# Performance work log

Measured on AMD Instinct MI355X. Metric: run time of the kernel, lower is better.

Reference implementation:

```python
import jax, jax.numpy as jnp
import numpy as np

N = 100000   # nodes
E = 300000   # directed edges
D = 256      # emb_dim
G = 4000     # graphs
L = 5        # num_layer
F_IN = 40    # num_atom_features
NUM_BOND_TYPE = 6       # pretrain-gnns convention; self-loop bond type = 4
NUM_BOND_DIRECTION = 3
EPS = 1e-5


def setup_inputs() -> dict:
    key = jax.random.key(0)
    ks = jax.random.split(key, 32)
    s = 0.05
    inp = {}
    inp["x"] = jax.random.normal(ks[0], (N, F_IN), jnp.float32)
    inp["edge_index"] = jax.random.randint(ks[1], (2, E), 0, N)
    inp["edge_attr"] = jax.random.randint(ks[2], (E, 2), 0, 3)
    inp["batch"] = jnp.sort(jax.random.randint(ks[3], (N,), 0, G))
    # atom embedding (Linear + ReLU)
    inp["embW"] = jax.random.normal(ks[4], (F_IN, D), jnp.float32) * s
    inp["embB"] = jnp.zeros((D,), jnp.float32)
    # per-layer GINConv params (stacked over layers)
    inp["ee1"] = jax.random.normal(ks[5], (L, NUM_BOND_TYPE, D), jnp.float32) * s
    inp["ee2"] = jax.random.normal(ks[6], (L, NUM_BOND_DIRECTION, D), jnp.float32) * s
    inp["W1"] = jax.random.normal(ks[7], (L, D, 2 * D), jnp.float32) * s
    inp["b1"] = jnp.zeros((L, 2 * D), jnp.float32)
    inp["W2"] = jax.random.normal(ks[8], (L, 2 * D, D), jnp.float32) * s
    inp["b2"] = jnp.zeros((L, D), jnp.float32)
    inp["bn_g"] = jnp.ones((L, D), jnp.float32)
    inp["bn_b"] = jnp.zeros((L, D), jnp.float32)
    # MLP head: 256 -> 256 -> 128 -> 64 -> 32 -> 1
    dims = [D, D, D // 2, D // 4, D // 8]
    kk = jax.random.split(ks[9], 5)
    for i in range(4):
        inp[f"hW{i}"] = jax.random.normal(kk[i], (dims[i], dims[i + 1]), jnp.float32) * s
        inp[f"hb{i}"] = jnp.zeros((dims[i + 1],), jnp.float32)
    inp["hWo"] = jax.random.normal(kk[4], (dims[4], 1), jnp.float32) * s
    inp["hbo"] = jnp.zeros((1,), jnp.float32)
    return inp


def reference(x, edge_index, edge_attr, batch, embW, embB, ee1, ee2, W1, b1, W2, b2,
              bn_g, bn_b, hW0, hb0, hW1, hb1, hW2, hb2, hW3, hb3, hWo, hbo):
    src, dst = edge_index[0], edge_index[1]
    ea0, ea1 = edge_attr[:, 0], edge_attr[:, 1]
    # x_embedding1: Linear + ReLU
    h = jax.nn.relu(x @ embW + embB)
    for l in range(L):
        # GINConv: gather source features + edge embeddings, scatter-add to dst
        msg = h[src] + ee1[l][ea0] + ee2[l][ea1]        # [E, D]
        agg = jax.ops.segment_sum(msg, dst, num_segments=N)
        # self-loop message (bond type 4, direction 0)
        agg = agg + h + ee1[l][4] + ee2[l][0]
        # GIN MLP: Linear(D, 2D) -> ReLU -> Linear(2D, D)
        h2 = jax.nn.relu(agg @ W1[l] + b1[l]) @ W2[l] + b2[l]
        # BatchNorm1d (training-mode batch statistics, biased variance)
        mu = h2.mean(axis=0)
        var = h2.var(axis=0)
        h2 = (h2 - mu) * jax.lax.rsqrt(var + EPS) * bn_g[l] + bn_b[l]
        if l < L - 1:
            h2 = jax.nn.relu(h2)
        # dropout with drop_ratio=0.0 -> identity
        h = h2
    # JK == 'last'
    node_rep = h
    # global_mean_pool
    counts = jnp.maximum(jax.ops.segment_sum(jnp.ones((N,), node_rep.dtype), batch, num_segments=G), 1.0)
    mol = jax.ops.segment_sum(node_rep, batch, num_segments=G) / counts[:, None]
    # MLP head
    z = jax.nn.relu(mol @ hW0 + hb0)
    z = jax.nn.relu(z @ hW1 + hb1)
    z = jax.nn.relu(z @ hW2 + hb2)
    z = jax.nn.relu(z @ hW3 + hb3)
    out = z @ hWo + hbo
    return out.reshape(-1)  # MolEmbed.view(-1), num_tasks == 1
```

## Files before the change

### kernel.cpp

```cpp
#include <hip/hip_runtime.h>
#include <hip/hip_bf16.h>

#define NN 100000
#define EE 300000
#define GG 4000
#define LL 5
#define GPB 4
#define SC_CHUNK 1024
#define SC_NB ((NN + SC_CHUNK - 1) / SC_CHUNK)

typedef _Float16 half8  __attribute__((ext_vector_type(8)));
typedef _Float16 half4v __attribute__((ext_vector_type(4)));
typedef float    f32x4  __attribute__((ext_vector_type(4)));

__device__ inline short f2h(float f) {
    _Float16 h = (_Float16)f;
    short s; __builtin_memcpy(&s, &h, 2); return s;
}

__device__ inline void async_load16(const void* g, void* l) {
    __builtin_amdgcn_global_load_lds(
        (const __attribute__((address_space(1))) unsigned int*)g,
        (__attribute__((address_space(3))) unsigned int*)l, 16, 0, 0);
}

__global__ __launch_bounds__(256) void k_count(
    int* __restrict__ deg, const int* __restrict__ ei)
{
    int e = blockIdx.x * 256 + threadIdx.x;
    if (e < EE) atomicAdd(&deg[ei[EE + e]], 1);
}

__global__ __launch_bounds__(256) void k_scan_partial(
    int* __restrict__ partial, const int* __restrict__ deg)
{
    int b = blockIdx.x, t = threadIdx.x;
    int lane = t & 63, w = t >> 6;
    int base = b * SC_CHUNK + t * 4;
    int s = 0;
#pragma unroll
    for (int j = 0; j < 4; ++j) {
        int i = base + j;
        if (i < NN) s += deg[i];
    }
#pragma unroll
    for (int off = 1; off < 64; off <<= 1) s += __shfl_xor(s, off, 64);
    __shared__ int ws[4];
    if (lane == 0) ws[w] = s;
    __syncthreads();
    if (t == 0) partial[b] = ws[0] + ws[1] + ws[2] + ws[3];
}

__global__ __launch_bounds__(128) void k_scan_base(
    int* __restrict__ bases, int* __restrict__ offs, const int* __restrict__ partial)
{
    int t = threadIdx.x;
    int lane = t & 63, w = t >> 6;
    int p = (t < SC_NB) ? partial[t] : 0;
    int x = p;
#pragma unroll
    for (int off = 1; off < 64; off <<= 1) {
        int nb = __shfl_up(x, off, 64);
        if (lane >= off) x += nb;
    }
    __shared__ int w0tot;
    if (t == 63) w0tot = x;
    __syncthreads();
    if (w == 1) x += w0tot;
    if (t < SC_NB) bases[t] = x - p;
    if (t == 0) offs[NN] = EE;
}

__global__ __launch_bounds__(256) void k_scan_final(
    int* __restrict__ offs, int* __restrict__ cursor,
    const int* __restrict__ deg, const int* __restrict__ bases)
{
    int b = blockIdx.x, t = threadIdx.x;
    int lane = t & 63, w = t >> 6;
    int base = b * SC_CHUNK + t * 4;
    int v[4], pre[4], run = 0;
#pragma unroll
    for (int j = 0; j < 4; ++j) {
        int i = base + j;
        v[j] = (i < NN) ? deg[i] : 0;
        pre[j] = run;
        run += v[j];
    }
    int x = run;
#pragma unroll
    for (int off = 1; off < 64; off <<= 1) {
        int nb = __shfl_up(x, off, 64);
        if (lane >= off) x += nb;
    }
    int tex = x - run;
    __shared__ int ws[4];
    if (lane == 63) ws[w] = x;
    __syncthreads();
    int woff = 0;
    for (int k = 0; k < 4; ++k) if (k < w) woff += ws[k];
    int tbase = bases[b] + woff + tex;
#pragma unroll
    for (int j = 0; j < 4; ++j) {
        int i = base + j;
        if (i < NN) { offs[i] = tbase + pre[j]; cursor[i] = tbase + pre[j]; }
    }
}

__global__ __launch_bounds__(256) void k_fill(
    int* __restrict__ csr, int* __restrict__ cursor,
    const int* __restrict__ ei, const int* __restrict__ ea)
{
    int e = blockIdx.x * 256 + threadIdx.x;
    if (e >= EE) return;
    int s = ei[e];
    int d = ei[EE + e];
    int c = ea[2 * e] * 3 + ea[2 * e + 1];
    int slot = atomicAdd(&cursor[d], 1);
    csr[slot] = s | (c << 20);
}

__global__ __launch_bounds__(256) void k_goffs(
    int* __restrict__ goffs, const int* __restrict__ batch)
{
    int n = blockIdx.x * 256 + threadIdx.x;
    if (n >= NN) return;
    int b = batch[n];
    int bp = (n == 0) ? -1 : batch[n - 1];
    for (int g = bp + 1; g <= b; ++g) goffs[g] = n;
    if (n == NN - 1)
        for (int g = b + 1; g <= GG; ++g) goffs[g] = NN;
}

__global__ __launch_bounds__(256) void k_combo(
    float* __restrict__ tbl, const float* __restrict__ ee1, const float* __restrict__ ee2)
{
    int c = blockIdx.x;
    int l = blockIdx.y;
    int t = threadIdx.x;
    int i1 = (c < 9) ? c / 3 : 4;
    int i2 = (c < 9) ? c % 3 : 0;
    tbl[((size_t)l * 10 + c) * 256 + t] =
        ee1[((size_t)l * 6 + i1) * 256 + t] + ee2[((size_t)l * 3 + i2) * 256 + t];
}

__global__ __launch_bounds__(256) void k_pack_emb(
    _Float16* __restrict__ Wep, const float* __restrict__ embW)
{
    int idx = blockIdx.x * 256 + threadIdx.x;
    int ks = idx >> 13, r = idx & 8191;
    int n = r >> 5, kk = r & 31;
    int k = ks * 32 + kk;
    float v = (k < 40) ? embW[(size_t)k * 256 + n] : 0.f;
    Wep[idx] = (_Float16)v;
}

__global__ __launch_bounds__(256) void k_embed_mfma(
    _Float16* __restrict__ H, const float* __restrict__ x,
    const _Float16* __restrict__ Wep, const float* __restrict__ bias)
{
    __shared__ __align__(16) char smem[67584];
    _Float16* As = (_Float16*)smem;
    _Float16* Bs = (_Float16*)(smem + 16384);
    _Float16* Cs = (_Float16*)smem;

    const int t = threadIdx.x;
    const int w = t >> 6, lane = t & 63;
    const int quad = lane >> 4, l16 = lane & 15;
    const int wr = w >> 1, wc = w & 1;
    const int gm0 = blockIdx.x * 128;

#pragma unroll
    for (int i = 0; i < 8; ++i) {
        int u = i * 256 + t;
        async_load16((const char*)Wep + u * 16, (char*)Bs + u * 16);
    }

    {
        int row = t >> 1, half = t & 1;
        int rg = gm0 + row; if (rg > NN - 1) rg = NN - 1;
        const float* xp = x + (size_t)rg * 40 + half * 20;
        float v[20];
#pragma unroll
        for (int j = 0; j < 5; ++j) {
            float4 q = *(const float4*)(xp + j * 4);
            v[j * 4 + 0] = q.x; v[j * 4 + 1] = q.y; v[j * 4 + 2] = q.z; v[j * 4 + 3] = q.w;
        }
#pragma unroll
        for (int j = 0; j < 20; ++j) {
            int col = half * 20 + j;
            int ks = col >> 5, kk = col & 31;
            As[ks * 4096 + row * 32 + kk] = (_Float16)v[j];
        }
        int kb = 8 + half * 12;
#pragma unroll
        for (int j = 0; j < 12; ++j)
            As[4096 + row * 32 + kb + j] = (_Float16)0.f;
    }

    float biasreg[8];
#pragma unroll
    for (int nt = 0; nt < 8; ++nt)
        biasreg[nt] = bias[wc * 128 + nt * 16 + l16];

    f32x4 acc[4][8];
#pragma unroll
    for (int i = 0; i < 4; ++i)
#pragma unroll
        for (int j = 0; j < 8; ++j) acc[i][j] = (f32x4){0.f, 0.f, 0.f, 0.f};

    __syncthreads();

#pragma unroll
    for (int ks = 0; ks < 2; ++ks) {
        half8 af[4], bfr[8];
#pragma unroll
        for (int mt = 0; mt < 4; ++mt)
            af[mt] = *(const half8*)(As + ks * 4096 + (wr * 64 + mt * 16 + l16) * 32 + quad * 8);
#pragma unroll
        for (int nt = 0; nt < 8; ++nt)
            bfr[nt] = *(const half8*)(Bs + ks * 8192 + (wc * 128 + nt * 16 + l16) * 32 + quad * 8);
#pragma unroll
        for (int mt = 0; mt < 4; ++mt)
#pragma unroll
            for (int nt = 0; nt < 8; ++nt)
                acc[mt][nt] = __builtin_amdgcn_mfma_f32_16x16x32_f16(
                    af[mt], bfr[nt], acc[mt][nt], 0, 0, 0);
    }

    __syncthreads();
#pragma unroll
    for (int mt = 0; mt < 4; ++mt)
#pragma unroll
        for (int nt = 0; nt < 8; ++nt)
#pragma unroll
            for (int r = 0; r < 4; ++r) {
                int row = wr * 64 + mt * 16 + quad * 4 + r;
                int col = wc * 128 + nt * 16 + l16;
                Cs[row * 264 + col] = (_Float16)fmaxf(acc[mt][nt][r] + biasreg[nt], 0.f);
            }
    __syncthreads();
#pragma unroll
    for (int i = 0; i < 16; ++i) {
        int u = i * 256 + t;
        int m = u >> 5, ch = u & 31;
        int grow = gm0 + m;
        if (grow < NN)
            *(int4*)(H + (size_t)grow * 256 + ch * 8) =
                *(const int4*)(Cs + m * 264 + ch * 8);
    }
}

template <int AFF>
__global__ __launch_bounds__(256) void k_aggregate(
    _Float16* __restrict__ agg, const _Float16* __restrict__ hin,
    const int* __restrict__ offs, const int* __restrict__ csr,
    const float* __restrict__ tbl,
    const float* __restrict__ scale, const float* __restrict__ shift)
{
    int t = threadIdx.x;
    int w = t >> 6, lane = t & 63;
    int n = blockIdx.x * 4 + w;

    f32x4 sc, sh;
    if (AFF) { sc = ((const f32x4*)scale)[lane]; sh = ((const f32x4*)shift)[lane]; }
    const f32x4* tb4 = (const f32x4*)tbl;

    half4v hv = *(const half4v*)(hin + (size_t)n * 256 + lane * 4);
    f32x4 acc = tb4[9 * 64 + lane];
#pragma unroll
    for (int i = 0; i < 4; ++i) {
        float v = (float)hv[i];
        if (AFF) v = fmaf(v, sc[i], sh[i]);
        acc[i] += fmaxf(v, 0.f);
    }

    int o0 = offs[n], o1 = offs[n + 1];
    for (int j = o0; j < o1; ++j) {
        int entry = csr[j];
        int s = entry & 0xFFFFF;
        int c = entry >> 20;
        half4v gv = *(const half4v*)(hin + (size_t)s * 256 + lane * 4);
        f32x4 tv = tb4[c * 64 + lane];
#pragma unroll
        for (int i = 0; i < 4; ++i) {
            float v = (float)gv[i];
            if (AFF) v = fmaf(v, sc[i], sh[i]);
            acc[i] += fmaxf(v, 0.f) + tv[i];
        }
    }

    half4v o;
#pragma unroll
    for (int i = 0; i < 4; ++i) o[i] = (_Float16)acc[i];
    *(half4v*)(agg + (size_t)n * 256 + lane * 4) = o;
}

__global__ __launch_bounds__(256) void k_pack(
    short* __restrict__ dst, const float* __restrict__ src, int K, int Nsz)
{
    int nb = blockIdx.x, kb = blockIdx.y, l = blockIdx.z;
    int t = threadIdx.x;
    __shared__ float T[32][65];
    const float* s = src + ((size_t)l * K + kb * 32) * Nsz + nb * 64;
#pragma unroll
    for (int i = 0; i < 8; ++i) {
        int idx = i * 256 + t;
        int kk = idx >> 6, nl = idx & 63;
        T[kk][nl] = s[(size_t)kk * Nsz + nl];
    }
    __syncthreads();
    int nl = t >> 2, kq = t & 3;
    union { short s[8]; int4 v; } o;
#pragma unroll
    for (int j = 0; j < 8; ++j) o.s[j] = f2h(T[kq * 8 + j][nl]);
    short* d = dst + (((size_t)l * (K / 32) + kb) * Nsz + nb * 64 + nl) * 32 + kq * 8;
    *(int4*)d = o.v;
}

__global__ __launch_bounds__(256) void k_fused_mlp(
    _Float16* __restrict__ H2, const _Float16* __restrict__ A,
    const short* __restrict__ W1p, const float* __restrict__ b1,
    const short* __restrict__ W2p, const float* __restrict__ b2,
    float* __restrict__ stats)
{
    __shared__ __align__(16) char smem[49152];
    _Float16* As = (_Float16*)smem;
    _Float16* Us = (_Float16*)(smem + 32768);
    _Float16* Cs = (_Float16*)smem;

    const int t = threadIdx.x;
    const int w = t >> 6, lane = t & 63;
    const int quad = lane >> 4, l16 = lane & 15;
    const int bm = blockIdx.x;
    const int gm0 = bm * 64;
    const int swz = l16 & 7;

#pragma unroll
    for (int i = 0; i < 8; ++i) {
        int u = i * 256 + t;
        int row = u >> 5;
        int gcol = (u & 31) ^ (row & 7);
        int grow = gm0 + row; if (grow > NN - 1) grow = NN - 1;
        async_load16(A + (size_t)grow * 256 + gcol * 8, (char*)As + u * 16);
    }

    f32x4 acc2[4][4];
#pragma unroll
    for (int i = 0; i < 4; ++i)
#pragma unroll
        for (int j = 0; j < 4; ++j) acc2[i][j] = (f32x4){0.f, 0.f, 0.f, 0.f};

    __syncthreads();

    for (int j = 0; j < 4; ++j) {
        f32x4 acc1[2][4];
#pragma unroll
        for (int a = 0; a < 2; ++a)
#pragma unroll
            for (int b = 0; b < 4; ++b) acc1[a][b] = (f32x4){0.f, 0.f, 0.f, 0.f};

#pragma unroll
        for (int kb = 0; kb < 8; ++kb) {
            half8 a1[2], b1f[4];
#pragma unroll
            for (int ct = 0; ct < 2; ++ct) {
                int uc = j * 128 + w * 32 + ct * 16 + l16;
                a1[ct] = *(const half8*)((const _Float16*)W1p +
                         ((size_t)kb * 512 + uc) * 32 + quad * 8);
            }
            int slotA = (kb * 4 + quad) ^ swz;
#pragma unroll
            for (int urt = 0; urt < 4; ++urt)
                b1f[urt] = *(const half8*)(As + (urt * 16 + l16) * 256 + slotA * 8);
#pragma unroll
            for (int ct = 0; ct < 2; ++ct)
#pragma unroll
                for (int urt = 0; urt < 4; ++urt)
                    acc1[ct][urt] = __builtin_amdgcn_mfma_f32_16x16x32_f16(
                        a1[ct], b1f[urt], acc1[ct][urt], 0, 0, 0);
        }

#pragma unroll
        for (int ct = 0; ct < 2; ++ct) {
            int ucl = w * 32 + ct * 16 + quad * 4;
            float4 bv = *(const float4*)(b1 + j * 128 + ucl);
            int G = ucl >> 3;
            int hs = quad & 1;
#pragma unroll
            for (int urt = 0; urt < 4; ++urt) {
                int ur = urt * 16 + l16;
                int S = G ^ (ur & 7);
                half4v o;
                o[0] = (_Float16)fmaxf(acc1[ct][urt][0] + bv.x, 0.f);
                o[1] = (_Float16)fmaxf(acc1[ct][urt][1] + bv.y, 0.f);
                o[2] = (_Float16)fmaxf(acc1[ct][urt][2] + bv.z, 0.f);
                o[3] = (_Float16)fmaxf(acc1[ct][urt][3] + bv.w, 0.f);
                *(half4v*)(Us + ur * 128 + S * 8 + hs * 4) = o;
            }
        }
        __syncthreads();

#pragma unroll
        for (int kk = 0; kk < 4; ++kk) {
            int kb2 = j * 4 + kk;
            half8 a2[4], b2f[4];
#pragma unroll
            for (int nt = 0; nt < 4; ++nt) {
                int n = w * 64 + nt * 16 + l16;
                a2[nt] = *(const half8*)((const _Float16*)W2p +
                         ((size_t)kb2 * 256 + n) * 32 + quad * 8);
            }
            int slotU = (kk * 4 + quad) ^ swz;
#pragma unroll
            for (int mt = 0; mt < 4; ++mt)
                b2f[mt] = *(const half8*)(Us + (mt * 16 + l16) * 128 + slotU * 8);
#pragma unroll
            for (int nt = 0; nt < 4; ++nt)
#pragma unroll
                for (int mt = 0; mt < 4; ++mt)
                    acc2[nt][mt] = __builtin_amdgcn_mfma_f32_16x16x32_f16(
                        a2[nt], b2f[mt], acc2[nt][mt], 0, 0, 0);
        }
        __syncthreads();
    }

    int slot2 = bm & 63;
#pragma unroll
    for (int nt = 0; nt < 4; ++nt) {
        int nb = w * 64 + nt * 16 + quad * 4;
        float4 bv = *(const float4*)(b2 + nb);
        float s1[4] = {0.f, 0.f, 0.f, 0.f};
        float s2[4] = {0.f, 0.f, 0.f, 0.f};
#pragma unroll
        for (int mt = 0; mt < 4; ++mt) {
            int mr = mt * 16 + l16;
            int m = gm0 + mr;
            float v0 = acc2[nt][mt][0] + bv.x;
            float v1 = acc2[nt][mt][1] + bv.y;
            float v2 = acc2[nt][mt][2] + bv.z;
            float v3 = acc2[nt][mt][3] + bv.w;
            half4v o;
            o[0] = (_Float16)v0; o[1] = (_Float16)v1;
            o[2] = (_Float16)v2; o[3] = (_Float16)v3;
            *(half4v*)(Cs + mr * 264 + nb) = o;
            if (m < NN) {
                s1[0] += v0; s1[1] += v1; s1[2] += v2; s1[3] += v3;
                s2[0] += v0 * v0; s2[1] += v1 * v1;
                s2[2] += v2 * v2; s2[3] += v3 * v3;
            }
        }
#pragma unroll
        for (int r = 0; r < 4; ++r) {
            s1[r] += __shfl_xor(s1[r], 1, 64); s2[r] += __shfl_xor(s2[r], 1, 64);
            s1[r] += __shfl_xor(s1[r], 2, 64); s2[r] += __shfl_xor(s2[r], 2, 64);
            s1[r] += __shfl_xor(s1[r], 4, 64); s2[r] += __shfl_xor(s2[r], 4, 64);
            s1[r] += __shfl_xor(s1[r], 8, 64); s2[r] += __shfl_xor(s2[r], 8, 64);
            if (l16 == 0) {
                atomicAdd(&stats[slot2 * 512 + nb + r], s1[r]);
                atomicAdd(&stats[slot2 * 512 + 256 + nb + r], s2[r]);
            }
        }
    }
    __syncthreads();
#pragma unroll
    for (int i = 0; i < 8; ++i) {
        int u = i * 256 + t;
        int m = u >> 5, ch = u & 31;
        int grow = gm0 + m;
        if (grow < NN)
            *(int4*)(H2 + (size_t)grow * 256 + ch * 8) =
                *(const int4*)(Cs + m * 264 + ch * 8);
    }
}

__global__ __launch_bounds__(256) void k_bn_finalize(
    float* __restrict__ scale, float* __restrict__ shift,
    float* __restrict__ stats,
    const float* __restrict__ bn_g, const float* __restrict__ bn_b)
{
    int t = threadIdx.x;
    float s1 = 0.f, s2 = 0.f;
    for (int j = 0; j < 64; ++j) {
        s1 += stats[j * 512 + t];
        s2 += stats[j * 512 + 256 + t];
        stats[j * 512 + t] = 0.f;
        stats[j * 512 + 256 + t] = 0.f;
    }
    float mu  = s1 / (float)NN;
    float var = s2 / (float)NN - mu * mu;
    float sc  = bn_g[t] * rsqrtf(var + 1e-5f);
    scale[t] = sc;
    shift[t] = bn_b[t] - mu * sc;
}

__global__ __launch_bounds__(256) void k_pool(
    float* __restrict__ mol, const _Float16* __restrict__ h,
    const int* __restrict__ goffs,
    const float* __restrict__ scale, const float* __restrict__ shift)
{
    int g = blockIdx.x;
    int t = threadIdx.x;
    int s = goffs[g], e = goffs[g + 1];
    float sum = 0.f;
    for (int n = s; n < e; ++n) sum += (float)h[(size_t)n * 256 + t];
    int c = e - s; if (c < 1) c = 1;
    mol[(size_t)g * 256 + t] = fmaf(sum / (float)c, scale[t], shift[t]);
}

__global__ __launch_bounds__(256) void k_head(
    float* __restrict__ out, const float* __restrict__ mol,
    const float* __restrict__ hW0, const float* __restrict__ hb0,
    const float* __restrict__ hW1, const float* __restrict__ hb1,
    const float* __restrict__ hW2, const float* __restrict__ hb2,
    const float* __restrict__ hW3, const float* __restrict__ hb3,
    const float* __restrict__ hWo, const float* __restrict__ hbo)
{
    __shared__ float za[GPB][256];
    __shared__ float zb[GPB][256];
    const int t = threadIdx.x;
    const int g0 = blockIdx.x * GPB;

#pragma unroll
    for (int g = 0; g < GPB; ++g)
        za[g][t] = mol[(size_t)(g0 + g) * 256 + t];
    __syncthreads();

    {
        float acc[GPB];
#pragma unroll
        for (int g = 0; g < GPB; ++g) acc[g] = 0.f;
        for (int k = 0; k < 256; ++k) {
            float w = hW0[k * 256 + t];
#pragma unroll
            for (int g = 0; g < GPB; ++g) acc[g] = fmaf(za[g][k], w, acc[g]);
        }
        float b = hb0[t];
#pragma unroll
        for (int g = 0; g < GPB; ++g) zb[g][t] = fmaxf(acc[g] + b, 0.f);
    }
    __syncthreads();

    if (t < 128) {
        float acc[GPB];
#pragma unroll
        for (int g = 0; g < GPB; ++g) acc[g] = 0.f;
        for (int k = 0; k < 256; ++k) {
            float w = hW1[k * 128 + t];
#pragma unroll
            for (int g = 0; g < GPB; ++g) acc[g] = fmaf(zb[g][k], w, acc[g]);
        }
        float b = hb1[t];
#pragma unroll
        for (int g = 0; g < GPB; ++g) za[g][t] = fmaxf(acc[g] + b, 0.f);
    }
    __syncthreads();

    if (t < 64) {
        float acc[GPB];
#pragma unroll
        for (int g = 0; g < GPB; ++g) acc[g] = 0.f;
        for (int k = 0; k < 128; ++k) {
            float w = hW2[k * 64 + t];
#pragma unroll
            for (int g = 0; g < GPB; ++g) acc[g] = fmaf(za[g][k], w, acc[g]);
        }
        float b = hb2[t];
#pragma unroll
        for (int g = 0; g < GPB; ++g) zb[g][t] = fmaxf(acc[g] + b, 0.f);
    }
    __syncthreads();

    if (t < 32) {
        float acc[GPB];
#pragma unroll
        for (int g = 0; g < GPB; ++g) acc[g] = 0.f;
        for (int k = 0; k < 64; ++k) {
            float w = hW3[k * 32 + t];
#pragma unroll
            for (int g = 0; g < GPB; ++g) acc[g] = fmaf(zb[g][k], w, acc[g]);
        }
        float b = hb3[t];
#pragma unroll
        for (int g = 0; g < GPB; ++g) za[g][t] = fmaxf(acc[g] + b, 0.f);
    }
    __syncthreads();

    if (t < GPB) {
        float s = hbo[0];
        for (int k = 0; k < 32; ++k) s = fmaf(za[t][k], hWo[k], s);
        out[g0 + t] = s;
    }
}

extern "C" void kernel_launch(void* const* d_in, const int* in_sizes, int n_in,
                              void* d_out, int out_size, void* d_ws, size_t ws_size,
                              hipStream_t stream)
{
    const float* x    = (const float*)d_in[0];
    const int*   ei   = (const int*)d_in[1];
    const int*   ea   = (const int*)d_in[2];
    const int*   batch= (const int*)d_in[3];
    const float* embW = (const float*)d_in[4];
    const float* embB = (const float*)d_in[5];
    const float* ee1  = (const float*)d_in[6];
    const float* ee2  = (const float*)d_in[7];
    const float* W1   = (const float*)d_in[8];
    const float* b1   = (const float*)d_in[9];
    const float* W2   = (const float*)d_in[10];
    const float* b2   = (const float*)d_in[11];
    const float* bng  = (const float*)d_in[12];
    const float* bnb  = (const float*)d_in[13];
    const float* hW0  = (const float*)d_in[14];
    const float* hb0  = (const float*)d_in[15];
    const float* hW1  = (const float*)d_in[16];
    const float* hb1  = (const float*)d_in[17];
    const float* hW2  = (const float*)d_in[18];
    const float* hb2  = (const float*)d_in[19];
    const float* hW3  = (const float*)d_in[20];
    const float* hb3  = (const float*)d_in[21];
    const float* hWo  = (const float*)d_in[22];
    const float* hbo  = (const float*)d_in[23];
    float* out = (float*)d_out;

    char* ws = (char*)d_ws;
    size_t off = 0;
    _Float16* h2buf = (_Float16*)(ws + off); off += (size_t)NN * 256 * 2;
    _Float16* aggbuf= (_Float16*)(ws + off); off += (size_t)NN * 256 * 2;
    short* W1p      = (short*)(ws + off);    off += (size_t)5 * 131072 * 2;
    short* W2p      = (short*)(ws + off);    off += (size_t)5 * 131072 * 2;
    _Float16* Wep   = (_Float16*)(ws + off); off += (size_t)2 * 8192 * 2;
    float* tbl      = (float*)(ws + off);    off += (size_t)5 * 10 * 256 * 4;
    float* stats    = (float*)(ws + off);    off += (size_t)64 * 512 * 4;
    float* scale    = (float*)(ws + off);    off += 256 * 4;
    float* shift    = (float*)(ws + off);    off += 256 * 4;
    float* mol      = (float*)(ws + off);    off += (size_t)GG * 256 * 4;
    int* deg        = (int*)(ws + off);      off += (size_t)NN * 4;
    int* offs       = (int*)(ws + off);      off += (size_t)(NN + 1) * 4;
    int* cursor     = (int*)(ws + off);      off += (size_t)NN * 4;
    int* csr        = (int*)(ws + off);      off += (size_t)EE * 4;
    int* goffs      = (int*)(ws + off);      off += (size_t)(GG + 1) * 4;
    int* partial    = (int*)(ws + off);      off += 128 * 4;
    int* bases      = (int*)(ws + off);      off += 128 * 4;

    hipMemsetAsync(deg, 0, (size_t)NN * 4, stream);
    hipMemsetAsync(stats, 0, (size_t)64 * 512 * 4, stream);
    k_count<<<(EE + 255) / 256, 256, 0, stream>>>(deg, ei);
    k_scan_partial<<<SC_NB, 256, 0, stream>>>(partial, deg);
    k_scan_base<<<1, 128, 0, stream>>>(bases, offs, partial);
    k_scan_final<<<SC_NB, 256, 0, stream>>>(offs, cursor, deg, bases);
    k_fill<<<(EE + 255) / 256, 256, 0, stream>>>(csr, cursor, ei, ea);
    k_goffs<<<(NN + 255) / 256, 256, 0, stream>>>(goffs, batch);
    k_combo<<<dim3(10, 5), 256, 0, stream>>>(tbl, ee1, ee2);
    k_pack<<<dim3(8, 8, 5), 256, 0, stream>>>(W1p, W1, 256, 512);
    k_pack<<<dim3(4, 16, 5), 256, 0, stream>>>(W2p, W2, 512, 256);
    k_pack_emb<<<64, 256, 0, stream>>>(Wep, embW);

    k_embed_mfma<<<782, 256, 0, stream>>>(h2buf, x, Wep, embB);

    const int FB = (NN + 63) / 64;
    for (int l = 0; l < LL; ++l) {
        if (l == 0)
            k_aggregate<0><<<NN / 4, 256, 0, stream>>>(aggbuf, h2buf, offs, csr,
                                                       tbl, scale, shift);
        else
            k_aggregate<1><<<NN / 4, 256, 0, stream>>>(aggbuf, h2buf, offs, csr,
                                                       tbl + (size_t)l * 10 * 256, scale, shift);
        k_fused_mlp<<<FB, 256, 0, stream>>>(h2buf, aggbuf,
                                            W1p + (size_t)l * 131072, b1 + l * 512,
                                            W2p + (size_t)l * 131072, b2 + l * 256, stats);
        k_bn_finalize<<<1, 256, 0, stream>>>(scale, shift, stats, bng + l * 256, bnb + l * 256);
    }

    k_pool<<<GG, 256, 0, stream>>>(mol, h2buf, goffs, scale, shift);
    k_head<<<GG / GPB, 256, 0, stream>>>(out, mol,
                                         hW0, hb0, hW1, hb1, hW2, hb2, hW3, hb3, hWo, hbo);
}
```

Before: 1.017 ms.

## Software-pipeline weight fragment loads and relax barriers in fused GIN MLP

Prefetches the W1 and W2 MFMA operand fragments from global memory one k-step ahead, using register double-buffering that carries across the j loop. This lets the global loads overlap the current MFMAs. It also replaces __syncthreads with an LDS-only waitcnt plus a raw barrier, so outstanding global prefetches are not drained at each barrier. A launch_bounds occupancy hint of 3 blocks per CU is added. In exchange the kernel holds more live registers, which may cause spills under the occupancy cap.

Measured after the change: 998.9 us. No clear change (-1.8%).

```diff
diff --git a/kernel.cpp b/kernel.cpp
--- a/kernel.cpp
+++ b/kernel.cpp
@@ -317,7 +317,7 @@
     *(int4*)d = o.v;
 }
 
-__global__ __launch_bounds__(256) void k_fused_mlp(
+__global__ __launch_bounds__(256, 3) void k_fused_mlp(
     _Float16* __restrict__ H2, const _Float16* __restrict__ A,
     const short* __restrict__ W1p, const float* __restrict__ b1,
     const short* __restrict__ W2p, const float* __restrict__ b2,
@@ -344,6 +344,14 @@
         async_load16(A + (size_t)grow * 256 + gcol * 8, (char*)As + u * 16);
     }
 
+    const _Float16* w1w = (const _Float16*)W1p + ((size_t)(w * 32 + l16)) * 32 + quad * 8;
+    const _Float16* w2w = (const _Float16*)W2p + ((size_t)(w * 64 + l16)) * 32 + quad * 8;
+
+    half8 a1p[2];
+#pragma unroll
+    for (int ct = 0; ct < 2; ++ct)
+        a1p[ct] = *(const half8*)(w1w + (size_t)(ct * 16) * 32);
+
     f32x4 acc2[4][4];
 #pragma unroll
     for (int i = 0; i < 4; ++i)
@@ -361,14 +369,16 @@
 
 #pragma unroll
         for (int kb = 0; kb < 8; ++kb) {
-            half8 a1[2], b1f[4];
-#pragma unroll
-            for (int ct = 0; ct < 2; ++ct) {
-                int uc = j * 128 + w * 32 + ct * 16 + l16;
-                a1[ct] = *(const half8*)((const _Float16*)W1p +
-                         ((size_t)kb * 512 + uc) * 32 + quad * 8);
+            half8 a1c[2];
+            a1c[0] = a1p[0]; a1c[1] = a1p[1];
+            if (kb < 7) {
+#pragma unroll
+                for (int ct = 0; ct < 2; ++ct)
+                    a1p[ct] = *(const half8*)(w1w +
+                        ((size_t)(kb + 1) * 512 + j * 128 + ct * 16) * 32);
             }
             int slotA = (kb * 4 + quad) ^ swz;
+            half8 b1f[4];
 #pragma unroll
             for (int urt = 0; urt < 4; ++urt)
                 b1f[urt] = *(const half8*)(As + (urt * 16 + l16) * 256 + slotA * 8);
@@ -377,8 +387,13 @@
 #pragma unroll
                 for (int urt = 0; urt < 4; ++urt)
                     acc1[ct][urt] = __builtin_amdgcn_mfma_f32_16x16x32_f16(
-                        a1[ct], b1f[urt], acc1[ct][urt], 0, 0, 0);
-        }
+                        a1c[ct], b1f[urt], acc1[ct][urt], 0, 0, 0);
+        }
+
+        half8 a2p[4];
+#pragma unroll
+        for (int nt = 0; nt < 4; ++nt)
+            a2p[nt] = *(const half8*)(w2w + ((size_t)(j * 4) * 256 + nt * 16) * 32);
 
 #pragma unroll
         for (int ct = 0; ct < 2; ++ct) {
@@ -398,19 +413,28 @@
                 *(half4v*)(Us + ur * 128 + S * 8 + hs * 4) = o;
             }
         }
-        __syncthreads();
+        asm volatile("s_waitcnt lgkmcnt(0)" ::: "memory");
+        __builtin_amdgcn_s_barrier();
+        __builtin_amdgcn_sched_barrier(0);
 
 #pragma unroll
         for (int kk = 0; kk < 4; ++kk) {
-            int kb2 = j * 4 + kk;
-            half8 a2[4], b2f[4];
-#pragma unroll
-            for (int nt = 0; nt < 4; ++nt) {
-                int n = w * 64 + nt * 16 + l16;
-                a2[nt] = *(const half8*)((const _Float16*)W2p +
-                         ((size_t)kb2 * 256 + n) * 32 + quad * 8);
+            half8 a2c[4];
+#pragma unroll
+            for (int nt = 0; nt < 4; ++nt) a2c[nt] = a2p[nt];
+            if (kk < 3) {
+#pragma unroll
+                for (int nt = 0; nt < 4; ++nt)
+                    a2p[nt] = *(const half8*)(w2w +
+                        ((size_t)(j * 4 + kk + 1) * 256 + nt * 16) * 32);
+            } else if (j < 3) {
+#pragma unroll
+                for (int ct = 0; ct < 2; ++ct)
+                    a1p[ct] = *(const half8*)(w1w +
+                        ((size_t)(j + 1) * 128 + ct * 16) * 32);
             }
             int slotU = (kk * 4 + quad) ^ swz;
+            half8 b2f[4];
 #pragma unroll
             for (int mt = 0; mt < 4; ++mt)
                 b2f[mt] = *(const half8*)(Us + (mt * 16 + l16) * 128 + slotU * 8);
@@ -419,9 +443,11 @@
 #pragma unroll
                 for (int mt = 0; mt < 4; ++mt)
                     acc2[nt][mt] = __builtin_amdgcn_mfma_f32_16x16x32_f16(
-                        a2[nt], b2f[mt], acc2[nt][mt], 0, 0, 0);
-        }
-        __syncthreads();
+                        a2c[nt], b2f[mt], acc2[nt][mt], 0, 0, 0);
+        }
+        asm volatile("s_waitcnt lgkmcnt(0)" ::: "memory");
+        __builtin_amdgcn_s_barrier();
+        __builtin_amdgcn_sched_barrier(0);
     }
 
     int slot2 = bm & 63;
```
